# Performance work log

Hardware: AMD Instinct MI355X
Metric: run time of the kernel (lower is better)

## Reference

```python
import jax, jax.numpy as jnp
import numpy as np

N_TOKEN = 267735
D = 512           # d_embed == d_proj
DIV = 4
CUTS = [0, 20000, 40000, 200000, 267735]  # cutoff_ends
N_TOKENS_BATCH = 1024  # len*bsz


def setup_inputs() -> dict:
    key = jax.random.key(0)
    ks = jax.random.split(key, 16)
    inp = {}
    inp["hidden"] = jax.random.normal(ks[0], (N_TOKENS_BATCH, D), jnp.float32)
    inp["target"] = jax.random.randint(ks[1], (N_TOKENS_BATCH,), 0, N_TOKEN)
    d_embs = [D // DIV ** i for i in range(4)]          # 512, 128, 32, 8
    sizes = [CUTS[i + 1] - CUTS[i] for i in range(4)]   # 20000, 20000, 160000, 67735
    for i in range(4):
        inp[f"W{i}"] = jax.random.normal(ks[2 + 3 * i], (sizes[i], d_embs[i]), jnp.float32) * (d_embs[i] ** -0.5)
        inp[f"b{i}"] = jax.random.normal(ks[3 + 3 * i], (sizes[i],), jnp.float32) * 0.01
        inp[f"proj{i}"] = jax.random.normal(ks[4 + 3 * i], (D, d_embs[i]), jnp.float32) * (D ** -0.5)
    inp["cluster_weight"] = jax.random.normal(ks[14], (3, D), jnp.float32) * (D ** -0.5)
    inp["cluster_bias"] = jax.random.normal(ks[15], (3,), jnp.float32) * 0.01
    return inp


def reference(hidden, target, W0, b0, proj0, W1, b1, proj1, W2, b2, proj2, W3, b3, proj3, cluster_weight, cluster_bias):
    n = jnp.arange(target.shape[0])
    # head = shortlist vocab + one logit per tail cluster
    head_w = jnp.concatenate([W0, cluster_weight], axis=0)   # [20003, D]
    head_b = jnp.concatenate([b0, cluster_bias], axis=0)     # [20003]
    head_logit = (hidden @ proj0) @ head_w.T + head_b        # einsum('bd,de,ev->bv')
    head_lp = jax.nn.log_softmax(head_logit, axis=-1)        # [N, 20003]
    head_size = head_lp.shape[1]
    # cluster id per token (0 = shortlist, 1..3 = tails)
    cid = ((target >= CUTS[1]).astype(jnp.int32)
           + (target >= CUTS[2]).astype(jnp.int32)
           + (target >= CUTS[3]).astype(jnp.int32))
    # shortlist: nll = -head_logprob[n, target]
    nll = -head_lp[n, jnp.clip(target, 0, CUTS[1] - 1)]
    for i, (Wi, bi, pi) in enumerate([(W1, b1, proj1), (W2, b2, proj2), (W3, b3, proj3)], start=1):
        l, r = CUTS[i], CUTS[i + 1]
        tail_lp = jax.nn.log_softmax((hidden @ pi) @ Wi.T + bi, axis=-1)  # [N, r-l]
        rel = jnp.clip(target - l, 0, r - l - 1)
        # faithful to original: head column indexed as head_logprob[:, -i]
        lp_i = head_lp[:, head_size - i] + tail_lp[n, rel]
        nll = jnp.where(cid == i, -lp_i, nll)
    return nll
```

## Files before the change

### kernel.cpp

```cpp
#include <hip/hip_runtime.h>

typedef short s16x8 __attribute__((ext_vector_type(8)));
typedef unsigned short u16x8 __attribute__((ext_vector_type(8)));
typedef float f32x4 __attribute__((ext_vector_type(4)));
typedef unsigned short ushort;

#define NTOK 1024
#define DHID 512

#define VH   20003
#define KH   512
#define NCH_H 80
#define TPC_H 16
#define VH_PAD 20480

#define V1   20000
#define K1   128
#define NCH_1 80
#define TPC_1 16
#define V1_PAD 20480

#define V2   160000
#define K2   32
#define NCH_2 128
#define TPC_2 80
#define V2_PAD 163840

#define V3   67735
#define K3   32
#define NCH_3 67
#define TPC_3 64
#define V3_PAD 68608

#define PAD_BIAS (-1e30f)

#define OFF_HW   0UL
#define OFF_W1   (OFF_HW  + (unsigned long)VH_PAD*KH*2)
#define OFF_W2   (OFF_W1  + (unsigned long)V1_PAD*K1*2)
#define OFF_W3   (OFF_W2  + (unsigned long)V2_PAD*K2*2)
#define OFF_HID  (OFF_W3  + (unsigned long)V3_PAD*K3*2)
#define OFF_PT0  (OFF_HID + (unsigned long)NTOK*DHID*2)
#define OFF_PT1  (OFF_PT0 + (unsigned long)512*DHID*2)
#define OFF_PT2  (OFF_PT1 + (unsigned long)128*DHID*2)
#define OFF_PT3  (OFF_PT2 + (unsigned long)32*DHID*2)
#define OFF_H0   (OFF_PT3 + (unsigned long)32*DHID*2)
#define OFF_H1   (OFF_H0  + (unsigned long)NTOK*512*2)
#define OFF_H2   (OFF_H1  + (unsigned long)NTOK*128*2)
#define OFF_H3   (OFF_H2  + (unsigned long)NTOK*32*2)
#define OFF_HB   (OFF_H3  + (unsigned long)NTOK*32*2)
#define OFF_B1   (OFF_HB  + (unsigned long)VH_PAD*4)
#define OFF_B2   (OFF_B1  + (unsigned long)V1_PAD*4)
#define OFF_B3   (OFF_B2  + (unsigned long)V2_PAD*4)
#define OFF_SH   (OFF_B3  + (unsigned long)V3_PAD*4)
#define OFF_S1   (OFF_SH  + (unsigned long)NTOK*NCH_H*4)
#define OFF_S2   (OFF_S1  + (unsigned long)NTOK*NCH_1*4)
#define OFF_S3   (OFF_S2  + (unsigned long)NTOK*NCH_2*4)

__device__ __forceinline__ ushort f2bf(float f) {
    union { float f; unsigned u; } x; x.f = f;
    unsigned r = x.u + 0x7fffu + ((x.u >> 16) & 1u);
    return (ushort)(r >> 16);
}
__device__ __forceinline__ float bf2f(ushort h) {
    union { unsigned u; float f; } x; x.u = ((unsigned)h) << 16;
    return x.f;
}
__device__ __forceinline__ f32x4 mfma_bf16(s16x8 a, s16x8 b, f32x4 c) {
    return __builtin_amdgcn_mfma_f32_16x16x32_bf16(a, b, c, 0, 0, 0);
}
__device__ __forceinline__ void ld8(const float* p, float* v) {
    float4 a = *(const float4*)p, b = *(const float4*)(p + 4);
    v[0]=a.x; v[1]=a.y; v[2]=a.z; v[3]=a.w; v[4]=b.x; v[5]=b.y; v[6]=b.z; v[7]=b.w;
}
__device__ __forceinline__ void gld_lds16(const ushort* g, ushort* l) {
    __builtin_amdgcn_global_load_lds(
        (const __attribute__((address_space(1))) unsigned int*)g,
        (__attribute__((address_space(3))) unsigned int*)l, 16, 0, 0);
}

#define WB_HW  20480L
#define WB_W1  5120L
#define WB_W2  10240L
#define WB_W3  4288L
#define WB_HID 1024L
#define WB_PT0 512L
#define WB_PT1 128L
#define WB_PT2 32L
#define WB_PT3 32L
#define WB_TOTAL (WB_HW+WB_W1+WB_W2+WB_W3+WB_HID+WB_PT0+WB_PT1+WB_PT2+WB_PT3)

__global__ __launch_bounds__(256) void prep_wswz(
    const float* __restrict__ hidden,
    const float* __restrict__ W0, const float* __restrict__ cw,
    const float* __restrict__ W1, const float* __restrict__ W2, const float* __restrict__ W3,
    const float* __restrict__ p0, const float* __restrict__ p1,
    const float* __restrict__ p2, const float* __restrict__ p3,
    ushort* __restrict__ hw, ushort* __restrict__ ow1,
    ushort* __restrict__ ow2, ushort* __restrict__ ow3,
    ushort* __restrict__ hid,
    ushort* __restrict__ pT0, ushort* __restrict__ pT1,
    ushort* __restrict__ pT2, ushort* __restrict__ pT3)
{
    int lane = threadIdx.x & 63;
    int r = lane & 15, quad = lane >> 4;
    long wb0 = (long)blockIdx.x * 4 + (threadIdx.x >> 6);
    long nw = (long)gridDim.x * 4;
    for (long wb = wb0; wb < WB_TOTAL; wb += nw) {
        long b = wb;
        float vals[8];
        #pragma unroll
        for (int j = 0; j < 8; ++j) vals[j] = 0.f;
        ushort* dst;
        if (b < WB_HW) {
            long tile = b >> 4, ks = b & 15;
            long v = tile * 16 + r, k = ks * 32 + quad * 8;
            if (v < 20000)      ld8(W0 + v * 512 + k, vals);
            else if (v < VH)    ld8(cw + (v - 20000) * 512 + k, vals);
            dst = hw + b * 512 + (long)lane * 8;
        } else if ((b -= WB_HW) < WB_W1) {
            long tile = b >> 2, ks = b & 3;
            long v = tile * 16 + r, k = ks * 32 + quad * 8;
            if (v < V1) ld8(W1 + v * 128 + k, vals);
            dst = ow1 + b * 512 + (long)lane * 8;
        } else if ((b -= WB_W1) < WB_W2) {
            long v = b * 16 + r;
            if (v < V2) ld8(W2 + v * 32 + quad * 8, vals);
            dst = ow2 + b * 512 + (long)lane * 8;
        } else if ((b -= WB_W2) < WB_W3) {
            long v = b * 16 + r;
            if (v < V3 && quad == 0) ld8(W3 + v * 8, vals);
            dst = ow3 + b * 512 + (long)lane * 8;
        } else if ((b -= WB_W3) < WB_HID) {
            long tile = b >> 4, ks = b & 15;
            long v = tile * 16 + r, k = ks * 32 + quad * 8;
            ld8(hidden + v * 512 + k, vals);
            dst = hid + b * 512 + (long)lane * 8;
        } else if ((b -= WB_HID) < WB_PT0) {
            long tile = b >> 4, ks = b & 15;
            long c = tile * 16 + r, k = ks * 32 + quad * 8;
            #pragma unroll
            for (int j = 0; j < 8; ++j) vals[j] = p0[(k + j) * 512 + c];
            dst = pT0 + b * 512 + (long)lane * 8;
        } else if ((b -= WB_PT0) < WB_PT1) {
            long tile = b >> 4, ks = b & 15;
            long c = tile * 16 + r, k = ks * 32 + quad * 8;
            #pragma unroll
            for (int j = 0; j < 8; ++j) vals[j] = p1[(k + j) * 128 + c];
            dst = pT1 + b * 512 + (long)lane * 8;
        } else if ((b -= WB_PT1) < WB_PT2) {
            long tile = b >> 4, ks = b & 15;
            long c = tile * 16 + r, k = ks * 32 + quad * 8;
            #pragma unroll
            for (int j = 0; j < 8; ++j) vals[j] = p2[(k + j) * 32 + c];
            dst = pT2 + b * 512 + (long)lane * 8;
        } else {
            b -= WB_PT2;
            long tile = b >> 4, ks = b & 15;
            long c = tile * 16 + r, k = ks * 32 + quad * 8;
            if (c < 8) {
                #pragma unroll
                for (int j = 0; j < 8; ++j) vals[j] = p3[(k + j) * 8 + c];
            }
            dst = pT3 + b * 512 + (long)lane * 8;
        }
        u16x8 o;
        #pragma unroll
        for (int j = 0; j < 8; ++j) o[j] = f2bf(vals[j]);
        *(u16x8*)dst = o;
    }
}

#define E_HB  ((long)VH_PAD)
#define E_B1  ((long)V1_PAD)
#define E_B2  ((long)V2_PAD)
#define E_B3  ((long)V3_PAD)
#define E_BIAS (E_HB+E_B1+E_B2+E_B3)

__global__ __launch_bounds__(256) void prep_bias(
    const float* __restrict__ b0, const float* __restrict__ b1,
    const float* __restrict__ b2, const float* __restrict__ b3,
    const float* __restrict__ cb,
    float* __restrict__ hbp, float* __restrict__ ob1,
    float* __restrict__ ob2, float* __restrict__ ob3)
{
    long stride = (long)gridDim.x * blockDim.x;
    for (long i = (long)blockIdx.x * blockDim.x + threadIdx.x; i < E_BIAS; i += stride) {
        long j = i;
        if (j < E_HB) {
            hbp[j] = (j < 20000) ? b0[j] : (j < VH) ? cb[j - 20000] : PAD_BIAS;
        } else if ((j -= E_HB) < E_B1) {
            ob1[j] = (j < V1) ? b1[j] : PAD_BIAS;
        } else if ((j -= E_B1) < E_B2) {
            ob2[j] = (j < V2) ? b2[j] : PAD_BIAS;
        } else { j -= E_B2;
            ob3[j] = (j < V3) ? b3[j] : PAD_BIAS;
        }
    }
}

__device__ __forceinline__ void gemm_body(
    const ushort* __restrict__ A, const ushort* __restrict__ Bt,
    ushort* __restrict__ Hout, int dpad, int c_tile)
{
    int wave = threadIdx.x >> 6, lane = threadIdx.x & 63;
    int quad = lane >> 4, colid = lane & 15;
    int m_tile = blockIdx.x * 4 + wave;
    const ushort* Ab = A + ((long)m_tile * 16) * 512 + lane * 8;
    const ushort* Bb = Bt + ((long)c_tile * 16) * 512 + lane * 8;
    f32x4 acc = {0.f, 0.f, 0.f, 0.f};
    #pragma unroll
    for (int ks = 0; ks < 16; ++ks) {
        s16x8 a = *(const s16x8*)(Ab + ks * 512);
        s16x8 b = *(const s16x8*)(Bb + ks * 512);
        acc = mfma_bf16(a, b, acc);
    }
    int KBo = dpad >> 5;
    int col = c_tile * 16 + colid;
    int ks_o = col >> 5, q_o = (col >> 3) & 3, j_o = col & 7;
    #pragma unroll
    for (int r = 0; r < 4; ++r) {
        int rm = quad * 4 + r;
        Hout[((long)m_tile * KBo + ks_o) * 512 + (q_o * 16 + rm) * 8 + j_o] = f2bf(acc[r]);
    }
}

__global__ __launch_bounds__(256) void gemm_all(
    const ushort* __restrict__ hid,
    const ushort* __restrict__ pT0, const ushort* __restrict__ pT1,
    const ushort* __restrict__ pT2, const ushort* __restrict__ pT3,
    ushort* __restrict__ H0, ushort* __restrict__ H1,
    ushort* __restrict__ H2, ushort* __restrict__ H3)
{
    int y = blockIdx.y;
    if (y < 32)      gemm_body(hid, pT0, H0, 512, y);
    else if (y < 40) gemm_body(hid, pT1, H1, 128, y - 32);
    else if (y < 42) gemm_body(hid, pT2, H2, 32,  y - 40);
    else             gemm_body(hid, pT3, H3, 32,  y - 42);
}


__device__ __forceinline__ void stage_grp16(const ushort* __restrict__ g,
                                            ushort* __restrict__ l,
                                            int wave, int lane)
{
    const ushort* gp = g + ((long)wave * 4) * 512 + lane * 8;
    ushort* lp = l + wave * 4 * 512;
    #pragma unroll
    for (int i = 0; i < 4; ++i) gld_lds16(gp + i * 512, lp + i * 512);
}

template<int KB>
__device__ __forceinline__ void compute_grp16(const ushort* __restrict__ buf,
                                              const s16x8 (&afrag)[KB],
                                              const float* __restrict__ ldsB,
                                              int tb0, int lane, int colid,
                                              float (&s_acc)[4])
{
    constexpr int TPG = 16 / KB;
    f32x4 acc0[TPG], acc1[TPG];
    #pragma unroll
    for (int t = 0; t < TPG; ++t) {
        acc0[t] = (f32x4){0.f, 0.f, 0.f, 0.f};
        acc1[t] = (f32x4){0.f, 0.f, 0.f, 0.f};
    }
    #pragma unroll
    for (int b = 0; b < 16; ++b) {
        s16x8 bb = *(const s16x8*)(buf + b * 512 + lane * 8);
        int t = b / KB, ks = b % KB;
        if ((KB > 1) && (ks & 1))
            acc1[t] = mfma_bf16(afrag[ks], bb, acc1[t]);
        else
            acc0[t] = mfma_bf16(afrag[ks], bb, acc0[t]);
    }
    #pragma unroll
    for (int t = 0; t < TPG; ++t) {
        float bval = ldsB[(tb0 + t) * 16 + colid];
        #pragma unroll
        for (int r = 0; r < 4; ++r) {
            float v = acc0[t][r];
            if (KB > 1) v += acc1[t][r];
            s_acc[r] += __expf(v + bval);
        }
    }
}

template<int KB>
__device__ __forceinline__ void fused_path(const ushort* __restrict__ A,
                                           const ushort* __restrict__ W,
                                           const float* __restrict__ bias,
                                           float* __restrict__ part_s,
                                           int tpc, int n_chunks, int chunk, int mblk,
                                           ushort* __restrict__ ldsW,
                                           float* __restrict__ ldsB)
{
    constexpr int TPG = 16 / KB;
    int wave = threadIdx.x >> 6, lane = threadIdx.x & 63;
    int quad = lane >> 4, colid = lane & 15;
    int m_tile = mblk * 4 + wave;
    long t0 = (long)chunk * tpc;
    const ushort* Wc = W + t0 * KB * 512;
    int ng = (tpc * KB) >> 4;

    s16x8 afrag[KB];
    const ushort* Ab = A + ((long)m_tile * KB) * 512 + lane * 8;
    #pragma unroll
    for (int ks = 0; ks < KB; ++ks) afrag[ks] = *(const s16x8*)(Ab + ks * 512);

    int nb = tpc * 16;
    for (int i = threadIdx.x; i < nb; i += 256) ldsB[i] = bias[t0 * 16 + i];
    __syncthreads();
    #pragma unroll
    for (int ks = 0; ks < KB; ++ks) asm volatile("" : "+v"(afrag[ks]));

    float s_acc[4] = {0.f, 0.f, 0.f, 0.f};

    stage_grp16(Wc, ldsW, wave, lane);
    stage_grp16(Wc + 16 * 512, ldsW + 16 * 512, wave, lane);

    for (int g = 0; g < ng - 1; ++g) {
        asm volatile("s_waitcnt vmcnt(4)" ::: "memory");
        __builtin_amdgcn_s_barrier();
        asm volatile("" ::: "memory");
        if (g + 2 < ng)
            stage_grp16(Wc + (long)(g + 2) * 16 * 512,
                        ldsW + ((g + 2) % 3) * (16 * 512), wave, lane);
        compute_grp16<KB>(ldsW + (g % 3) * (16 * 512), afrag, ldsB,
                          g * TPG, lane, colid, s_acc);
        asm volatile("s_waitcnt lgkmcnt(0)" ::: "memory");
    }
    asm volatile("s_waitcnt vmcnt(0)" ::: "memory");
    __builtin_amdgcn_s_barrier();
    asm volatile("" ::: "memory");
    compute_grp16<KB>(ldsW + ((ng - 1) % 3) * (16 * 512), afrag, ldsB,
                      (ng - 1) * TPG, lane, colid, s_acc);

    #pragma unroll
    for (int r = 0; r < 4; ++r) {
        float v = s_acc[r];
        v += __shfl_xor(v, 1);
        v += __shfl_xor(v, 2);
        v += __shfl_xor(v, 4);
        v += __shfl_xor(v, 8);
        s_acc[r] = v;
    }
    if (colid == 0) {
        #pragma unroll
        for (int r = 0; r < 4; ++r) {
            int m = m_tile * 16 + quad * 4 + r;
            part_s[(long)m * n_chunks + chunk] = s_acc[r];
        }
    }
}

__global__ __launch_bounds__(256, 3) void fused_all(
    const ushort* __restrict__ H0, const ushort* __restrict__ hw,
    const float* __restrict__ hbp, float* __restrict__ sH,
    const ushort* __restrict__ H1, const ushort* __restrict__ w1,
    const float* __restrict__ b1p, float* __restrict__ s1,
    const ushort* __restrict__ H2, const ushort* __restrict__ w2,
    const float* __restrict__ b2p, float* __restrict__ s2,
    const ushort* __restrict__ H3, const ushort* __restrict__ w3,
    const float* __restrict__ b3p, float* __restrict__ s3)
{
    __shared__ __align__(16) ushort ldsW[3 * 16 * 512];
    __shared__ float ldsB[1280];
    int id = blockIdx.x;
    int k = id & 7, s = id >> 3;
    int c = (s >> 4) * 8 + k;
    int mblk = s & 15;
    if (c >= 355) return;
    if (c < 80)       fused_path<16>(H0, hw, hbp, sH, TPC_H, NCH_H, c,       mblk, ldsW, ldsB);
    else if (c < 160) fused_path<4>(H1, w1, b1p, s1, TPC_1, NCH_1, c - 80,  mblk, ldsW, ldsB);
    else if (c < 288) fused_path<1>(H2, w2, b2p, s2, TPC_2, NCH_2, c - 160, mblk, ldsW, ldsB);
    else              fused_path<1>(H3, w3, b3p, s3, TPC_3, NCH_3, c - 288, mblk, ldsW, ldsB);
}

__device__ __forceinline__ float swz_dot(const ushort* __restrict__ H, int m,
                                         const ushort* __restrict__ Wm, long vrow,
                                         int K, int lane)
{
    float d = 0.f;
    if (lane * 8 < K) {
        int ks = lane >> 2, q = lane & 3;
        int KB = K >> 5;
        const ushort* hp = H + ((long)(m >> 4) * KB + ks) * 512 + (q * 16 + (m & 15)) * 8;
        const ushort* wp = Wm + ((vrow >> 4) * KB + ks) * 512 + (q * 16 + (int)(vrow & 15)) * 8;
        #pragma unroll
        for (int j = 0; j < 8; ++j) d += bf2f(hp[j]) * bf2f(wp[j]);
    }
    d += __shfl_xor(d, 1);  d += __shfl_xor(d, 2);  d += __shfl_xor(d, 4);
    d += __shfl_xor(d, 8);  d += __shfl_xor(d, 16); d += __shfl_xor(d, 32);
    return d;
}

__global__ __launch_bounds__(256) void finalize_kernel(
    const int* __restrict__ target,
    const ushort* __restrict__ H0, const ushort* __restrict__ hw,
    const float* __restrict__ hbp, const float* __restrict__ sH,
    const ushort* __restrict__ H1, const ushort* __restrict__ w1,
    const float* __restrict__ b1p, const float* __restrict__ s1,
    const ushort* __restrict__ H2, const ushort* __restrict__ w2,
    const float* __restrict__ b2p, const float* __restrict__ s2,
    const ushort* __restrict__ H3, const ushort* __restrict__ w3,
    const float* __restrict__ b3p, const float* __restrict__ s3,
    float* __restrict__ out)
{
    int wave = threadIdx.x >> 6, lane = threadIdx.x & 63;
    int m = blockIdx.x * 4 + wave;
    int t = target[m];
    int cid = (t >= 20000) + (t >= 40000) + (t >= 200000);

    float s = 0.f;
    for (int i = lane; i < NCH_H; i += 64) s += sH[(long)m * NCH_H + i];
    s += __shfl_xor(s, 1);  s += __shfl_xor(s, 2);  s += __shfl_xor(s, 4);
    s += __shfl_xor(s, 8);  s += __shfl_xor(s, 16); s += __shfl_xor(s, 32);
    float lse_h = __logf(s);

    int hc = (cid == 0) ? t : (20003 - cid);
    float d = swz_dot(H0, m, hw, hc, 512, lane);
    float nll = lse_h - (d + hbp[hc]);

    if (cid > 0) {
        const ushort *Hi, *Wi; const float *bi, *si; int K, nc, l;
        if (cid == 1)      { Hi = H1; Wi = w1; bi = b1p; si = s1; K = 128; nc = NCH_1; l = 20000; }
        else if (cid == 2) { Hi = H2; Wi = w2; bi = b2p; si = s2; K = 32;  nc = NCH_2; l = 40000; }
        else               { Hi = H3; Wi = w3; bi = b3p; si = s3; K = 32;  nc = NCH_3; l = 200000; }
        int rel = t - l;
        float ts = 0.f;
        for (int i = lane; i < nc; i += 64) ts += si[(long)m * nc + i];
        ts += __shfl_xor(ts, 1);  ts += __shfl_xor(ts, 2);  ts += __shfl_xor(ts, 4);
        ts += __shfl_xor(ts, 8);  ts += __shfl_xor(ts, 16); ts += __shfl_xor(ts, 32);
        float lse_t = __logf(ts);
        float dt = swz_dot(Hi, m, Wi, rel, K, lane);
        nll += lse_t - (dt + bi[rel]);
    }
    if (lane == 0) out[m] = nll;
}

extern "C" void kernel_launch(void* const* d_in, const int* in_sizes, int n_in,
                              void* d_out, int out_size, void* d_ws, size_t ws_size,
                              hipStream_t stream) {
    const float* hidden = (const float*)d_in[0];
    const int*   target = (const int*)d_in[1];
    const float* W0 = (const float*)d_in[2];
    const float* b0 = (const float*)d_in[3];
    const float* p0 = (const float*)d_in[4];
    const float* W1 = (const float*)d_in[5];
    const float* b1 = (const float*)d_in[6];
    const float* p1 = (const float*)d_in[7];
    const float* W2 = (const float*)d_in[8];
    const float* b2 = (const float*)d_in[9];
    const float* p2 = (const float*)d_in[10];
    const float* W3 = (const float*)d_in[11];
    const float* b3 = (const float*)d_in[12];
    const float* p3 = (const float*)d_in[13];
    const float* cw = (const float*)d_in[14];
    const float* cb = (const float*)d_in[15];

    char* ws = (char*)d_ws;
    ushort* hw  = (ushort*)(ws + OFF_HW);
    ushort* ow1 = (ushort*)(ws + OFF_W1);
    ushort* ow2 = (ushort*)(ws + OFF_W2);
    ushort* ow3 = (ushort*)(ws + OFF_W3);
    ushort* hid = (ushort*)(ws + OFF_HID);
    ushort* pT0 = (ushort*)(ws + OFF_PT0);
    ushort* pT1 = (ushort*)(ws + OFF_PT1);
    ushort* pT2 = (ushort*)(ws + OFF_PT2);
    ushort* pT3 = (ushort*)(ws + OFF_PT3);
    ushort* H0  = (ushort*)(ws + OFF_H0);
    ushort* H1  = (ushort*)(ws + OFF_H1);
    ushort* H2  = (ushort*)(ws + OFF_H2);
    ushort* H3  = (ushort*)(ws + OFF_H3);
    float* hbp = (float*)(ws + OFF_HB);
    float* b1p = (float*)(ws + OFF_B1);
    float* b2p = (float*)(ws + OFF_B2);
    float* b3p = (float*)(ws + OFF_B3);
    float* sH  = (float*)(ws + OFF_SH);
    float* s1  = (float*)(ws + OFF_S1);
    float* s2  = (float*)(ws + OFF_S2);
    float* s3  = (float*)(ws + OFF_S3);

    prep_wswz<<<10464, 256, 0, stream>>>(hidden, W0, cw, W1, W2, W3,
                                         p0, p1, p2, p3,
                                         hw, ow1, ow2, ow3, hid, pT0, pT1, pT2, pT3);
    prep_bias<<<1072, 256, 0, stream>>>(b0, b1, b2, b3, cb, hbp, b1p, b2p, b3p);

    gemm_all<<<dim3(NTOK / 64, 44), 256, 0, stream>>>(hid, pT0, pT1, pT2, pT3,
                                                      H0, H1, H2, H3);

    fused_all<<<5760, 256, 0, stream>>>(H0, hw, hbp, sH,
                                        H1, ow1, b1p, s1,
                                        H2, ow2, b2p, s2,
                                        H3, ow3, b3p, s3);

    finalize_kernel<<<NTOK / 4, 256, 0, stream>>>(target,
        H0, hw, hbp, sH, H1, ow1, b1p, s1, H2, ow2, b2p, s2, H3, ow3, b3p, s3,
        (float*)d_out);
}
```

Baseline: 254.0 us.

## Register-block multiple M tiles per wave, fold log2e into weights, rebalance grid

Each wave now keeps MREP row-tiles of A in registers, so every weight tile staged in LDS feeds several MFMAs. This cuts LDS and global weight traffic per output. Weights and biases are pre-scaled by log2(e) so the softmax sums use exp2 directly, and the bias is folded into the accumulator init. The block-to-work mapping is rewritten with a new balanced linearization, and the launch shrinks from 5760 to 1740 blocks. The extra accumulators raise register pressure, and pre-scaling in bf16 adds a small precision change.

```diff
diff --git a/kernel.cpp b/kernel.cpp
--- a/kernel.cpp
+++ b/kernel.cpp
@@ -33,6 +33,8 @@
 #define V3_PAD 68608
 
 #define PAD_BIAS (-1e30f)
+#define LOG2E 1.4426950408889634f
+#define LN2F  0.6931471805599453f
 
 #define OFF_HW   0UL
 #define OFF_W1   (OFF_HW  + (unsigned long)VH_PAD*KH*2)
@@ -110,6 +112,7 @@
         float vals[8];
         #pragma unroll
         for (int j = 0; j < 8; ++j) vals[j] = 0.f;
+        float scale = LOG2E;
         ushort* dst;
         if (b < WB_HW) {
             long tile = b >> 4, ks = b & 15;
@@ -131,29 +134,34 @@
             if (v < V3 && quad == 0) ld8(W3 + v * 8, vals);
             dst = ow3 + b * 512 + (long)lane * 8;
         } else if ((b -= WB_W3) < WB_HID) {
+            scale = 1.f;
             long tile = b >> 4, ks = b & 15;
             long v = tile * 16 + r, k = ks * 32 + quad * 8;
             ld8(hidden + v * 512 + k, vals);
             dst = hid + b * 512 + (long)lane * 8;
         } else if ((b -= WB_HID) < WB_PT0) {
+            scale = 1.f;
             long tile = b >> 4, ks = b & 15;
             long c = tile * 16 + r, k = ks * 32 + quad * 8;
             #pragma unroll
             for (int j = 0; j < 8; ++j) vals[j] = p0[(k + j) * 512 + c];
             dst = pT0 + b * 512 + (long)lane * 8;
         } else if ((b -= WB_PT0) < WB_PT1) {
+            scale = 1.f;
             long tile = b >> 4, ks = b & 15;
             long c = tile * 16 + r, k = ks * 32 + quad * 8;
             #pragma unroll
             for (int j = 0; j < 8; ++j) vals[j] = p1[(k + j) * 128 + c];
             dst = pT1 + b * 512 + (long)lane * 8;
         } else if ((b -= WB_PT1) < WB_PT2) {
+            scale = 1.f;
             long tile = b >> 4, ks = b & 15;
             long c = tile * 16 + r, k = ks * 32 + quad * 8;
             #pragma unroll
             for (int j = 0; j < 8; ++j) vals[j] = p2[(k + j) * 32 + c];
             dst = pT2 + b * 512 + (long)lane * 8;
         } else {
+            scale = 1.f;
             b -= WB_PT2;
             long tile = b >> 4, ks = b & 15;
             long c = tile * 16 + r, k = ks * 32 + quad * 8;
@@ -165,7 +173,7 @@
         }
         u16x8 o;
         #pragma unroll
-        for (int j = 0; j < 8; ++j) o[j] = f2bf(vals[j]);
+        for (int j = 0; j < 8; ++j) o[j] = f2bf(vals[j] * scale);
         *(u16x8*)dst = o;
     }
 }
@@ -187,13 +195,13 @@
     for (long i = (long)blockIdx.x * blockDim.x + threadIdx.x; i < E_BIAS; i += stride) {
         long j = i;
         if (j < E_HB) {
-            hbp[j] = (j < 20000) ? b0[j] : (j < VH) ? cb[j - 20000] : PAD_BIAS;
+            hbp[j] = ((j < 20000) ? b0[j] : (j < VH) ? cb[j - 20000] : PAD_BIAS) * LOG2E;
         } else if ((j -= E_HB) < E_B1) {
-            ob1[j] = (j < V1) ? b1[j] : PAD_BIAS;
+            ob1[j] = ((j < V1) ? b1[j] : PAD_BIAS) * LOG2E;
         } else if ((j -= E_B1) < E_B2) {
-            ob2[j] = (j < V2) ? b2[j] : PAD_BIAS;
+            ob2[j] = ((j < V2) ? b2[j] : PAD_BIAS) * LOG2E;
         } else { j -= E_B2;
-            ob3[j] = (j < V3) ? b3[j] : PAD_BIAS;
+            ob3[j] = ((j < V3) ? b3[j] : PAD_BIAS) * LOG2E;
         }
     }
 }
@@ -238,117 +246,139 @@
     else             gemm_body(hid, pT3, H3, 32,  y - 42);
 }
 
-
-__device__ __forceinline__ void stage_grp16(const ushort* __restrict__ g,
-                                            ushort* __restrict__ l,
-                                            int wave, int lane)
-{
-    const ushort* gp = g + ((long)wave * 4) * 512 + lane * 8;
-    ushort* lp = l + wave * 4 * 512;
-    #pragma unroll
-    for (int i = 0; i < 4; ++i) gld_lds16(gp + i * 512, lp + i * 512);
-}
-
-template<int KB>
-__device__ __forceinline__ void compute_grp16(const ushort* __restrict__ buf,
-                                              const s16x8 (&afrag)[KB],
-                                              const float* __restrict__ ldsB,
-                                              int tb0, int lane, int colid,
-                                              float (&s_acc)[4])
-{
-    constexpr int TPG = 16 / KB;
-    f32x4 acc0[TPG], acc1[TPG];
-    #pragma unroll
-    for (int t = 0; t < TPG; ++t) {
-        acc0[t] = (f32x4){0.f, 0.f, 0.f, 0.f};
-        acc1[t] = (f32x4){0.f, 0.f, 0.f, 0.f};
-    }
-    #pragma unroll
-    for (int b = 0; b < 16; ++b) {
+template<int TG>
+__device__ __forceinline__ void stage_grp(const ushort* __restrict__ g,
+                                          ushort* __restrict__ l,
+                                          int wave, int lane)
+{
+    constexpr int LPW = TG / 4;
+    const ushort* gp = g + ((long)wave * LPW) * 512 + lane * 8;
+    ushort* lp = l + wave * LPW * 512;
+    #pragma unroll
+    for (int i = 0; i < LPW; ++i) gld_lds16(gp + i * 512, lp + i * 512);
+}
+
+template<int KB, int MREP, int TG>
+__device__ __forceinline__ void compute_grp(const ushort* __restrict__ buf,
+                                            const s16x8 (&afrag)[MREP][KB],
+                                            const float* __restrict__ ldsB,
+                                            int tb0, int lane, int colid,
+                                            float (&s_acc)[MREP][4])
+{
+    constexpr int TPG = TG / KB;
+    f32x4 acc0[TPG][MREP];
+    f32x4 acc1[(KB > 1) ? TPG : 1][(KB > 1) ? MREP : 1];
+    float bv[TPG];
+    #pragma unroll
+    for (int t = 0; t < TPG; ++t) bv[t] = ldsB[(tb0 + t) * 16 + colid];
+    #pragma unroll
+    for (int t = 0; t < TPG; ++t)
+        #pragma unroll
+        for (int i = 0; i < MREP; ++i) {
+            acc0[t][i] = (f32x4){bv[t], bv[t], bv[t], bv[t]};
+            if (KB > 1) acc1[t][i] = (f32x4){0.f, 0.f, 0.f, 0.f};
+        }
+    #pragma unroll
+    for (int b = 0; b < TG; ++b) {
         s16x8 bb = *(const s16x8*)(buf + b * 512 + lane * 8);
         int t = b / KB, ks = b % KB;
-        if ((KB > 1) && (ks & 1))
-            acc1[t] = mfma_bf16(afrag[ks], bb, acc1[t]);
-        else
-            acc0[t] = mfma_bf16(afrag[ks], bb, acc0[t]);
-    }
-    #pragma unroll
-    for (int t = 0; t < TPG; ++t) {
-        float bval = ldsB[(tb0 + t) * 16 + colid];
-        #pragma unroll
-        for (int r = 0; r < 4; ++r) {
-            float v = acc0[t][r];
-            if (KB > 1) v += acc1[t][r];
-            s_acc[r] += __expf(v + bval);
+        #pragma unroll
+        for (int i = 0; i < MREP; ++i) {
+            if ((KB > 1) && (ks & 1))
+                acc1[t][i] = mfma_bf16(afrag[i][ks], bb, acc1[t][i]);
+            else
+                acc0[t][i] = mfma_bf16(afrag[i][ks], bb, acc0[t][i]);
         }
     }
-}
-
-template<int KB>
-__device__ __forceinline__ void fused_path(const ushort* __restrict__ A,
-                                           const ushort* __restrict__ W,
-                                           const float* __restrict__ bias,
-                                           float* __restrict__ part_s,
-                                           int tpc, int n_chunks, int chunk, int mblk,
-                                           ushort* __restrict__ ldsW,
-                                           float* __restrict__ ldsB)
-{
-    constexpr int TPG = 16 / KB;
+    #pragma unroll
+    for (int t = 0; t < TPG; ++t)
+        #pragma unroll
+        for (int i = 0; i < MREP; ++i)
+            #pragma unroll
+            for (int r = 0; r < 4; ++r) {
+                float v = acc0[t][i][r];
+                if (KB > 1) v += acc1[t][i][r];
+                s_acc[i][r] += __builtin_amdgcn_exp2f(v);
+            }
+}
+
+template<int KB, int MREP, int TG>
+__device__ __forceinline__ void fused_path(
+    const ushort* __restrict__ A, const ushort* __restrict__ W,
+    const float* __restrict__ bias, float* __restrict__ part_s,
+    int tpc, int n_chunks, int chunk, int mblk,
+    ushort* __restrict__ ldsW, float* __restrict__ ldsB)
+{
+    constexpr int TPG = TG / KB;
+    constexpr int LPW = TG / 4;
+    constexpr int BUFE = TG * 512;
     int wave = threadIdx.x >> 6, lane = threadIdx.x & 63;
     int quad = lane >> 4, colid = lane & 15;
-    int m_tile = mblk * 4 + wave;
+    int mt0 = mblk * (4 * MREP) + wave * MREP;
     long t0 = (long)chunk * tpc;
     const ushort* Wc = W + t0 * KB * 512;
-    int ng = (tpc * KB) >> 4;
-
-    s16x8 afrag[KB];
-    const ushort* Ab = A + ((long)m_tile * KB) * 512 + lane * 8;
-    #pragma unroll
-    for (int ks = 0; ks < KB; ++ks) afrag[ks] = *(const s16x8*)(Ab + ks * 512);
-
+    const int ng = (tpc * KB) / TG;
+
+    s16x8 afrag[MREP][KB];
+    #pragma unroll
+    for (int i = 0; i < MREP; ++i) {
+        const ushort* Ab = A + ((long)(mt0 + i) * KB) * 512 + lane * 8;
+        #pragma unroll
+        for (int ks = 0; ks < KB; ++ks) afrag[i][ks] = *(const s16x8*)(Ab + ks * 512);
+    }
     int nb = tpc * 16;
     for (int i = threadIdx.x; i < nb; i += 256) ldsB[i] = bias[t0 * 16 + i];
     __syncthreads();
     #pragma unroll
-    for (int ks = 0; ks < KB; ++ks) asm volatile("" : "+v"(afrag[ks]));
-
-    float s_acc[4] = {0.f, 0.f, 0.f, 0.f};
-
-    stage_grp16(Wc, ldsW, wave, lane);
-    stage_grp16(Wc + 16 * 512, ldsW + 16 * 512, wave, lane);
+    for (int i = 0; i < MREP; ++i)
+        #pragma unroll
+        for (int ks = 0; ks < KB; ++ks) asm volatile("" : "+v"(afrag[i][ks]));
+
+    float s_acc[MREP][4];
+    #pragma unroll
+    for (int i = 0; i < MREP; ++i)
+        #pragma unroll
+        for (int r = 0; r < 4; ++r) s_acc[i][r] = 0.f;
+
+    stage_grp<TG>(Wc, ldsW, wave, lane);
+    stage_grp<TG>(Wc + BUFE, ldsW + BUFE, wave, lane);
 
     for (int g = 0; g < ng - 1; ++g) {
-        asm volatile("s_waitcnt vmcnt(4)" ::: "memory");
+        if constexpr (LPW == 1)      asm volatile("s_waitcnt vmcnt(1)" ::: "memory");
+        else if constexpr (LPW == 2) asm volatile("s_waitcnt vmcnt(2)" ::: "memory");
+        else                         asm volatile("s_waitcnt vmcnt(4)" ::: "memory");
         __builtin_amdgcn_s_barrier();
-        asm volatile("" ::: "memory");
         if (g + 2 < ng)
-            stage_grp16(Wc + (long)(g + 2) * 16 * 512,
-                        ldsW + ((g + 2) % 3) * (16 * 512), wave, lane);
-        compute_grp16<KB>(ldsW + (g % 3) * (16 * 512), afrag, ldsB,
-                          g * TPG, lane, colid, s_acc);
+            stage_grp<TG>(Wc + (long)(g + 2) * BUFE,
+                          ldsW + ((g + 2) % 3) * BUFE, wave, lane);
+        compute_grp<KB, MREP, TG>(ldsW + (g % 3) * BUFE, afrag, ldsB,
+                                  g * TPG, lane, colid, s_acc);
         asm volatile("s_waitcnt lgkmcnt(0)" ::: "memory");
     }
     asm volatile("s_waitcnt vmcnt(0)" ::: "memory");
     __builtin_amdgcn_s_barrier();
-    asm volatile("" ::: "memory");
-    compute_grp16<KB>(ldsW + ((ng - 1) % 3) * (16 * 512), afrag, ldsB,
-                      (ng - 1) * TPG, lane, colid, s_acc);
-
-    #pragma unroll
-    for (int r = 0; r < 4; ++r) {
-        float v = s_acc[r];
-        v += __shfl_xor(v, 1);
-        v += __shfl_xor(v, 2);
-        v += __shfl_xor(v, 4);
-        v += __shfl_xor(v, 8);
-        s_acc[r] = v;
-    }
+    compute_grp<KB, MREP, TG>(ldsW + ((ng - 1) % 3) * BUFE, afrag, ldsB,
+                              (ng - 1) * TPG, lane, colid, s_acc);
+
+    #pragma unroll
+    for (int i = 0; i < MREP; ++i)
+        #pragma unroll
+        for (int r = 0; r < 4; ++r) {
+            float v = s_acc[i][r];
+            v += __shfl_xor(v, 1);
+            v += __shfl_xor(v, 2);
+            v += __shfl_xor(v, 4);
+            v += __shfl_xor(v, 8);
+            s_acc[i][r] = v;
+        }
     if (colid == 0) {
         #pragma unroll
-        for (int r = 0; r < 4; ++r) {
-            int m = m_tile * 16 + quad * 4 + r;
-            part_s[(long)m * n_chunks + chunk] = s_acc[r];
-        }
+        for (int i = 0; i < MREP; ++i)
+            #pragma unroll
+            for (int r = 0; r < 4; ++r) {
+                int m = (mt0 + i) * 16 + quad * 4 + r;
+                part_s[(long)m * n_chunks + chunk] = s_acc[i][r];
+            }
     }
 }
 
@@ -364,15 +394,21 @@
 {
     __shared__ __align__(16) ushort ldsW[3 * 16 * 512];
     __shared__ float ldsB[1280];
-    int id = blockIdx.x;
-    int k = id & 7, s = id >> 3;
-    int c = (s >> 4) * 8 + k;
-    int mblk = s & 15;
-    if (c >= 355) return;
-    if (c < 80)       fused_path<16>(H0, hw, hbp, sH, TPC_H, NCH_H, c,       mblk, ldsW, ldsB);
-    else if (c < 160) fused_path<4>(H1, w1, b1p, s1, TPC_1, NCH_1, c - 80,  mblk, ldsW, ldsB);
-    else if (c < 288) fused_path<1>(H2, w2, b2p, s2, TPC_2, NCH_2, c - 160, mblk, ldsW, ldsB);
-    else              fused_path<1>(H3, w3, b3p, s3, TPC_3, NCH_3, c - 288, mblk, ldsW, ldsB);
+    int bid = blockIdx.x;
+    int k = bid & 7, j = bid >> 3;
+    int L = k * 217 + (k < 4 ? k : 4) + j;
+    if (L < 640) {
+        fused_path<16, 2, 16>(H0, hw, hbp, sH, TPC_H, NCH_H, L >> 3, L & 7, ldsW, ldsB);
+    } else if (L < 960) {
+        int t = L - 640;
+        fused_path<4, 4, 8>(H1, w1, b1p, s1, TPC_1, NCH_1, t >> 2, t & 3, ldsW, ldsB);
+    } else if (L < 1472) {
+        int t = L - 960;
+        fused_path<1, 4, 4>(H2, w2, b2p, s2, TPC_2, NCH_2, t >> 2, t & 3, ldsW, ldsB);
+    } else {
+        int t = L - 1472;
+        fused_path<1, 4, 4>(H3, w3, b3p, s3, TPC_3, NCH_3, t >> 2, t & 3, ldsW, ldsB);
+    }
 }
 
 __device__ __forceinline__ float swz_dot(const ushort* __restrict__ H, int m,
@@ -418,7 +454,7 @@
 
     int hc = (cid == 0) ? t : (20003 - cid);
     float d = swz_dot(H0, m, hw, hc, 512, lane);
-    float nll = lse_h - (d + hbp[hc]);
+    float nll = lse_h - (d + hbp[hc]) * LN2F;
 
     if (cid > 0) {
         const ushort *Hi, *Wi; const float *bi, *si; int K, nc, l;
@@ -432,7 +468,7 @@
         ts += __shfl_xor(ts, 8);  ts += __shfl_xor(ts, 16); ts += __shfl_xor(ts, 32);
         float lse_t = __logf(ts);
         float dt = swz_dot(Hi, m, Wi, rel, K, lane);
-        nll += lse_t - (dt + bi[rel]);
+        nll += lse_t - (dt + bi[rel]) * LN2F;
     }
     if (lane == 0) out[m] = nll;
 }
@@ -488,7 +524,7 @@
     gemm_all<<<dim3(NTOK / 64, 44), 256, 0, stream>>>(hid, pT0, pT1, pT2, pT3,
                                                       H0, H1, H2, H3);
 
-    fused_all<<<5760, 256, 0, stream>>>(H0, hw, hbp, sH,
+    fused_all<<<1740, 256, 0, stream>>>(H0, hw, hbp, sH,
                                         H1, ow1, b1p, s1,
                                         H2, ow2, b2p, s2,
                                         H3, ow3, b3p, s3);
```

New measurement: 230.7 us. 9.2% less time.
